# Kernel optimization log

Hardware: AMD Instinct MI355X
Metric: run time of the kernel (lower is better)

The kernel has to match this reference:

```python
import jax, jax.numpy as jnp
import numpy as np
import math

B, T, D, H = 4, 2048, 1024, 16
DH = D // H

def setup_inputs() -> dict:
    key = jax.random.key(0)
    ks = jax.random.split(key, 5)
    scale = 1.0 / math.sqrt(D)
    x = jax.random.normal(ks[0], (B, T, D), dtype=jnp.float32)
    Wq = jax.random.normal(ks[1], (D, D), dtype=jnp.float32) * scale
    Wk = jax.random.normal(ks[2], (D, D), dtype=jnp.float32) * scale
    Wv = jax.random.normal(ks[3], (D, D), dtype=jnp.float32) * scale
    Wo = jax.random.normal(ks[4], (D, D), dtype=jnp.float32) * scale
    mask = jnp.tril(jnp.ones((T, T), dtype=jnp.int32))  # causal, 1=keep
    return {"x": x, "mask": mask, "Wq": Wq, "Wk": Wk, "Wv": Wv, "Wo": Wo}

def reference(x, mask, Wq, Wk, Wv, Wo):
    Bx, Tx, Dx = x.shape
    # nn.Linear(bias=False): y = x @ W.T
    q = (x @ Wq.T).reshape(Bx, Tx, H, DH).transpose(0, 2, 1, 3)  # [B,H,T,dh]
    k = (x @ Wk.T).reshape(Bx, Tx, H, DH).transpose(0, 2, 1, 3)
    v = (x @ Wv.T).reshape(Bx, Tx, H, DH).transpose(0, 2, 1, 3)
    scores = jnp.einsum('bhqd,bhkd->bhqk', q, k) / math.sqrt(DH)
    m = mask[None, None, :, :]  # [1,1,T,T]
    scores = scores + (m == 0).astype(scores.dtype) * -1e9
    attn = jax.nn.softmax(scores, axis=-1)  # stable (max-subtract) like original
    out = jnp.einsum('bhqk,bhkd->bhqd', attn, v)
    out = out.transpose(0, 2, 1, 3).reshape(Bx, Tx, Dx)
    return out @ Wo.T
```

## Files before the change

### kernel.cpp

```cpp
#include <hip/hip_runtime.h>
#include <stdint.h>

#define B_  4
#define T_  2048
#define D_  1024
#define H_  16
#define DH_ 64

typedef unsigned short u16;
typedef __attribute__((ext_vector_type(8))) short bf16x8;
typedef __attribute__((ext_vector_type(8))) unsigned short u16x8;
typedef __attribute__((ext_vector_type(4))) unsigned short u16x4;
typedef __attribute__((ext_vector_type(4))) float f32x4;

#define NT_ ((size_t)B_ * T_ * D_)
#define QSCALE 0.18033688011112043f

__device__ __forceinline__ u16 f2bf(float f) {
    union { float f; uint32_t u; } v; v.f = f;
    uint32_t r = v.u + 0x7FFFu + ((v.u >> 16) & 1u);
    return (u16)(r >> 16);
}

__device__ __forceinline__ uint32_t pack2(float lo, float hi) {
    union { float f; uint32_t u; } a, b; a.f = lo; b.f = hi;
    return __builtin_amdgcn_perm(b.u, a.u, 0x07060302u);
}

__device__ __forceinline__ void gl2lds16(const u16* g, u16* l) {
    __builtin_amdgcn_global_load_lds(
        (const __attribute__((address_space(1))) unsigned int*)g,
        (__attribute__((address_space(3))) unsigned int*)l,
        16, 0, 0);
}

__global__ __launch_bounds__(256) void cvt_x_kernel(
    const float* __restrict__ src, u16* __restrict__ dst, int n8)
{
    int i = blockIdx.x * 256 + threadIdx.x;
    if (i >= n8) return;
    f32x4 a = ((const f32x4*)src)[2 * i];
    f32x4 b = ((const f32x4*)src)[2 * i + 1];
    u16x8 o;
    o[0]=f2bf(a[0]); o[1]=f2bf(a[1]); o[2]=f2bf(a[2]); o[3]=f2bf(a[3]);
    o[4]=f2bf(b[0]); o[5]=f2bf(b[1]); o[6]=f2bf(b[2]); o[7]=f2bf(b[3]);
    ((u16x8*)dst)[i] = o;
}

__global__ __launch_bounds__(256) void cvt_w_kernel(
    const float* __restrict__ w0, const float* __restrict__ w1,
    const float* __restrict__ w2, const float* __restrict__ w3,
    u16* __restrict__ dst)
{
    const float* src = (blockIdx.y == 0) ? w0 : (blockIdx.y == 1) ? w1
                     : (blockIdx.y == 2) ? w2 : w3;
    u16* d = dst + (size_t)blockIdx.y * (D_ * D_);
    int i = blockIdx.x * 256 + threadIdx.x;
    f32x4 a = ((const f32x4*)src)[2 * i];
    f32x4 b = ((const f32x4*)src)[2 * i + 1];
    u16x8 o;
    o[0]=f2bf(a[0]); o[1]=f2bf(a[1]); o[2]=f2bf(a[2]); o[3]=f2bf(a[3]);
    o[4]=f2bf(b[0]); o[5]=f2bf(b[1]); o[6]=f2bf(b[2]); o[7]=f2bf(b[3]);
    ((u16x8*)d)[i] = o;
}

template<int OUT_MODE>
__global__ __launch_bounds__(256) void gemm_bt_kernel(
    const u16* __restrict__ X, const u16* __restrict__ W,
    void* __restrict__ C, int M, int N, int K)
{
    __shared__ __align__(16) u16 As[128 * 64];
    __shared__ __align__(16) u16 Bs[128 * 64];

    const int tid  = threadIdx.x;
    const int wave = tid >> 6;
    const int lane = tid & 63;
    const int lq = lane >> 4;
    const int lm = lane & 15;
    const int m0 = blockIdx.x * 128;
    const int n0 = blockIdx.y * 128;
    const int wm = (wave & 1) * 64;
    const int wn = (wave >> 1) * 64;

    f32x4 acc[4][4] = {};

    const int r0 = wave * 32 + (lane >> 3);
    const int c0 = (lane & 7) * 8;
    const u16* gA = X + (size_t)(m0 + r0) * K + c0;
    const u16* gB = W + (size_t)(n0 + r0) * K + c0;
    u16* lA = As + wave * 32 * 64;
    u16* lB = Bs + wave * 32 * 64;

    for (int k0 = 0; k0 < K; k0 += 64) {
#pragma unroll
        for (int p = 0; p < 4; ++p) {
            gl2lds16(gA + (size_t)p * 8 * K + k0, lA + p * 8 * 64);
            gl2lds16(gB + (size_t)p * 8 * K + k0, lB + p * 8 * 64);
        }
        __syncthreads();
#pragma unroll
        for (int ks = 0; ks < 2; ++ks) {
            bf16x8 af[4], bfr[4];
#pragma unroll
            for (int t = 0; t < 4; ++t)
                af[t] = *(const bf16x8*)(As + (wm + t * 16 + lm) * 64 + ks * 32 + lq * 8);
#pragma unroll
            for (int t = 0; t < 4; ++t)
                bfr[t] = *(const bf16x8*)(Bs + (wn + t * 16 + lm) * 64 + ks * 32 + lq * 8);
#pragma unroll
            for (int i = 0; i < 4; ++i)
#pragma unroll
                for (int j = 0; j < 4; ++j)
                    acc[i][j] = __builtin_amdgcn_mfma_f32_16x16x32_bf16(
                        af[i], bfr[j], acc[i][j], 0, 0, 0);
        }
        __syncthreads();
    }

    const int region = n0 >> 10;
#pragma unroll
    for (int i = 0; i < 4; ++i)
#pragma unroll
        for (int j = 0; j < 4; ++j) {
            int rowb = m0 + wm + i * 16 + lq * 4;
            int col  = n0 + wn + j * 16 + lm;
            if (OUT_MODE == 2) {
#pragma unroll
                for (int r = 0; r < 4; ++r)
                    ((float*)C)[(size_t)(rowb + r) * N + col] = acc[i][j][r];
            } else {
                u16* Qp = (u16*)C;
                int colr = col & 1023;
                if (region == 0) {
#pragma unroll
                    for (int r = 0; r < 4; ++r)
                        Qp[(size_t)(rowb + r) * D_ + colr] = f2bf(acc[i][j][r] * QSCALE);
                } else if (region == 1) {
#pragma unroll
                    for (int r = 0; r < 4; ++r)
                        (Qp + NT_)[(size_t)(rowb + r) * D_ + colr] = f2bf(acc[i][j][r]);
                } else {
                    int b = rowb >> 11, t = rowb & (T_ - 1);
                    u16x4 pk;
#pragma unroll
                    for (int r = 0; r < 4; ++r) pk[r] = f2bf(acc[i][j][r]);
                    *(u16x4*)((Qp + 2 * NT_) + ((size_t)b * D_ + colr) * T_ + t) = pk;
                }
            }
        }
}

__global__ __launch_bounds__(64) void attn_kernel(
    const u16* __restrict__ Qg, const u16* __restrict__ Kg,
    const u16* __restrict__ Vtg, u16* __restrict__ Og)
{
    __shared__ __align__(16) u16 Pl[64 * 132];

    const int lane = threadIdx.x;
    const int lq = lane >> 4, lm = lane & 15;
    const int id = blockIdx.x;
    const int xs = id & 7;
    const int k8 = id >> 3;
    const int bh = xs + 8 * (k8 & 7);
    const int pi = k8 >> 3;
    const int b = bh >> 4, h = bh & 15;

    const size_t batchoff = (size_t)b * T_ * D_;
    const size_t headoff  = (size_t)h * DH_;
    const size_t vbase    = (size_t)bh * DH_ * T_;

#pragma unroll 1
    for (int ph = 0; ph < 2; ++ph) {
        const int qj  = ph ? (31 - pi) : pi;
        const int qw  = qj * 64;
        const int ktd = qj >> 1;
        const int odd = qj & 1;

        bf16x8 aq[4][2];
#pragma unroll
        for (int qf = 0; qf < 4; ++qf) {
            const u16* qrow = Qg + batchoff + (size_t)(qw + qf * 16 + lm) * D_ + headoff;
            aq[qf][0] = *(const bf16x8*)(qrow + lq * 8);
            aq[qf][1] = *(const bf16x8*)(qrow + 32 + lq * 8);
        }

        f32x4 oaccT[4][4] = {};
        float l_lane[4] = {0.f, 0.f, 0.f, 0.f};

#pragma unroll 1
        for (int kt = 0; kt <= ktd; ++kt) {
            const bool diag = (kt == ktd);
            const int ksmax = diag ? (odd ? 3 : 1) : 3;

#pragma unroll
            for (int c = 0; c < 4; ++c) {
                if (c <= ksmax) {
#pragma unroll
                    for (int t = 0; t < 2; ++t) {
                        const int mt = 2 * c + t;
                        const u16* krow = Kg + batchoff
                            + (size_t)(kt * 128 + mt * 16 + lm) * D_ + headoff;
                        bf16x8 kf0 = *(const bf16x8*)(krow + lq * 8);
                        bf16x8 kf1 = *(const bf16x8*)(krow + 32 + lq * 8);
                        f32x4 s[4];
#pragma unroll
                        for (int qf = 0; qf < 4; ++qf) {
                            s[qf] = f32x4{0.f, 0.f, 0.f, 0.f};
                            s[qf] = __builtin_amdgcn_mfma_f32_16x16x32_bf16(
                                kf0, aq[qf][0], s[qf], 0, 0, 0);
                            s[qf] = __builtin_amdgcn_mfma_f32_16x16x32_bf16(
                                kf1, aq[qf][1], s[qf], 0, 0, 0);
                        }
                        if (diag) {
                            int keyb = kt * 128 + mt * 16 + lq * 4;
#pragma unroll
                            for (int qf = 0; qf < 4; ++qf) {
                                int query = qw + qf * 16 + lm;
#pragma unroll
                                for (int r = 0; r < 4; ++r)
                                    if (keyb + r > query) s[qf][r] = -1e9f;
                            }
                        }
#pragma unroll
                        for (int qf = 0; qf < 4; ++qf) {
                            float p0 = __builtin_amdgcn_exp2f(s[qf][0]);
                            float p1 = __builtin_amdgcn_exp2f(s[qf][1]);
                            float p2 = __builtin_amdgcn_exp2f(s[qf][2]);
                            float p3 = __builtin_amdgcn_exp2f(s[qf][3]);
                            l_lane[qf] += (p0 + p1) + (p2 + p3);
                            uint2 d; d.x = pack2(p0, p1); d.y = pack2(p2, p3);
                            *(uint2*)(Pl + (qf * 16 + lm) * 132 + mt * 16 + lq * 4) = d;
                        }
                    }

                    bf16x8 pf[4];
#pragma unroll
                    for (int qf = 0; qf < 4; ++qf)
                        pf[qf] = *(const bf16x8*)(Pl + (qf * 16 + lm) * 132 + c * 32 + lq * 8);
#pragma unroll
                    for (int mo = 0; mo < 4; ++mo) {
                        const u16* vrow = Vtg + vbase
                            + (size_t)(mo * 16 + lm) * T_ + kt * 128 + c * 32;
                        bf16x8 vf = *(const bf16x8*)(vrow + lq * 8);
#pragma unroll
                        for (int qf = 0; qf < 4; ++qf)
                            oaccT[qf][mo] = __builtin_amdgcn_mfma_f32_16x16x32_bf16(
                                vf, pf[qf], oaccT[qf][mo], 0, 0, 0);
                    }
                }
            }
        }

#pragma unroll
        for (int qf = 0; qf < 4; ++qf) {
            float l = l_lane[qf];
            l += __shfl_xor(l, 16, 64);
            l += __shfl_xor(l, 32, 64);
            float inv = 1.0f / l;
            int row = qw + qf * 16 + lm;
            u16* obase = Og + batchoff + (size_t)row * D_ + headoff;
#pragma unroll
            for (int mo = 0; mo < 4; ++mo) {
                uint2 d;
                d.x = pack2(oaccT[qf][mo][0] * inv, oaccT[qf][mo][1] * inv);
                d.y = pack2(oaccT[qf][mo][2] * inv, oaccT[qf][mo][3] * inv);
                *(uint2*)(obase + mo * 16 + lq * 4) = d;
            }
        }
    }
}

extern "C" void kernel_launch(void* const* d_in, const int* in_sizes, int n_in,
                              void* d_out, int out_size, void* d_ws, size_t ws_size,
                              hipStream_t stream)
{
    const float* x  = (const float*)d_in[0];
    const float* Wq = (const float*)d_in[2];
    const float* Wk = (const float*)d_in[3];
    const float* Wv = (const float*)d_in[4];
    const float* Wo = (const float*)d_in[5];

    const size_t DD = (size_t)D_ * D_;
    u16* Qb  = (u16*)d_ws;
    u16* Kb  = Qb + NT_;
    u16* Vb  = Kb + NT_;
    u16* Ob  = Vb + NT_;
    u16* xb  = Ob + NT_;
    u16* wb  = xb + NT_;

    const int M = B_ * T_;

    cvt_x_kernel<<<dim3((int)(NT_ / 8 / 256)), 256, 0, stream>>>(x, xb, (int)(NT_ / 8));
    cvt_w_kernel<<<dim3((int)(DD / 8 / 256), 4), 256, 0, stream>>>(Wq, Wk, Wv, Wo, wb);

    gemm_bt_kernel<3><<<dim3(M / 128, 3 * D_ / 128), 256, 0, stream>>>(
        xb, wb, Qb, M, 3 * D_, D_);

    attn_kernel<<<dim3(1024), 64, 0, stream>>>(Qb, Kb, Vb, Ob);

    gemm_bt_kernel<2><<<dim3(M / 128, D_ / 128), 256, 0, stream>>>(
        Ob, wb + 3 * DD, d_out, M, D_, D_);
}
```

Measured before the change: 319.5 us.

## Split attention key tiles across two waves per block with LDS reduction

Each attention block now uses two waves that process alternating 128-key tiles for the same 64-query tile, then combine partial output accumulators and row sums through shared memory before normalizing and writing. The P staging buffer is shrunk to a per-wave 32-column slice. This doubles the parallelism per query tile and shortens the serial key loop, in exchange for extra LDS traffic, two barriers per phase, and more shared memory per block. It relies on the fixed-max softmax, where no running max is kept, so partial sums can simply be added.

```diff
diff --git a/kernel.cpp b/kernel.cpp
--- a/kernel.cpp
+++ b/kernel.cpp
@@ -150,13 +150,17 @@
         }
 }
 
-__global__ __launch_bounds__(64) void attn_kernel(
+__global__ __launch_bounds__(128) void attn_kernel(
     const u16* __restrict__ Qg, const u16* __restrict__ Kg,
     const u16* __restrict__ Vtg, u16* __restrict__ Og)
 {
-    __shared__ __align__(16) u16 Pl[64 * 132];
-
-    const int lane = threadIdx.x;
+    __shared__ __align__(16) u16 Pl[2 * 64 * 40];
+    __shared__ __align__(16) float Oc[16 * 64 * 4];
+    __shared__ __align__(16) float Lc[4 * 64];
+
+    const int tid  = threadIdx.x;
+    const int wave = tid >> 6;
+    const int lane = tid & 63;
     const int lq = lane >> 4, lm = lane & 15;
     const int id = blockIdx.x;
     const int xs = id & 7;
@@ -169,6 +173,8 @@
     const size_t headoff  = (size_t)h * DH_;
     const size_t vbase    = (size_t)bh * DH_ * T_;
 
+    u16* pw = Pl + wave * 64 * 40;
+
 #pragma unroll 1
     for (int ph = 0; ph < 2; ++ph) {
         const int qj  = ph ? (31 - pi) : pi;
@@ -188,7 +194,7 @@
         float l_lane[4] = {0.f, 0.f, 0.f, 0.f};
 
 #pragma unroll 1
-        for (int kt = 0; kt <= ktd; ++kt) {
+        for (int kt = wave; kt <= ktd; kt += 2) {
             const bool diag = (kt == ktd);
             const int ksmax = diag ? (odd ? 3 : 1) : 3;
 
@@ -229,14 +235,14 @@
                             float p3 = __builtin_amdgcn_exp2f(s[qf][3]);
                             l_lane[qf] += (p0 + p1) + (p2 + p3);
                             uint2 d; d.x = pack2(p0, p1); d.y = pack2(p2, p3);
-                            *(uint2*)(Pl + (qf * 16 + lm) * 132 + mt * 16 + lq * 4) = d;
+                            *(uint2*)(pw + (qf * 16 + lm) * 40 + t * 16 + lq * 4) = d;
                         }
                     }
 
                     bf16x8 pf[4];
 #pragma unroll
                     for (int qf = 0; qf < 4; ++qf)
-                        pf[qf] = *(const bf16x8*)(Pl + (qf * 16 + lm) * 132 + c * 32 + lq * 8);
+                        pf[qf] = *(const bf16x8*)(pw + (qf * 16 + lm) * 40 + lq * 8);
 #pragma unroll
                     for (int mo = 0; mo < 4; ++mo) {
                         const u16* vrow = Vtg + vbase
@@ -251,22 +257,45 @@
             }
         }
 
-#pragma unroll
-        for (int qf = 0; qf < 4; ++qf) {
-            float l = l_lane[qf];
-            l += __shfl_xor(l, 16, 64);
-            l += __shfl_xor(l, 32, 64);
-            float inv = 1.0f / l;
-            int row = qw + qf * 16 + lm;
-            u16* obase = Og + batchoff + (size_t)row * D_ + headoff;
-#pragma unroll
-            for (int mo = 0; mo < 4; ++mo) {
-                uint2 d;
-                d.x = pack2(oaccT[qf][mo][0] * inv, oaccT[qf][mo][1] * inv);
-                d.y = pack2(oaccT[qf][mo][2] * inv, oaccT[qf][mo][3] * inv);
-                *(uint2*)(obase + mo * 16 + lq * 4) = d;
-            }
-        }
+        if (wave == 1) {
+#pragma unroll
+            for (int qf = 0; qf < 4; ++qf) {
+#pragma unroll
+                for (int mo = 0; mo < 4; ++mo)
+                    *(f32x4*)&Oc[((qf * 4 + mo) * 64 + lane) * 4] = oaccT[qf][mo];
+                Lc[qf * 64 + lane] = l_lane[qf];
+            }
+        }
+        __syncthreads();
+        if (wave == 0) {
+#pragma unroll
+            for (int qf = 0; qf < 4; ++qf) {
+#pragma unroll
+                for (int mo = 0; mo < 4; ++mo) {
+                    f32x4 o = *(const f32x4*)&Oc[((qf * 4 + mo) * 64 + lane) * 4];
+#pragma unroll
+                    for (int r = 0; r < 4; ++r) oaccT[qf][mo][r] += o[r];
+                }
+                l_lane[qf] += Lc[qf * 64 + lane];
+            }
+#pragma unroll
+            for (int qf = 0; qf < 4; ++qf) {
+                float l = l_lane[qf];
+                l += __shfl_xor(l, 16, 64);
+                l += __shfl_xor(l, 32, 64);
+                float inv = 1.0f / l;
+                int row = qw + qf * 16 + lm;
+                u16* obase = Og + batchoff + (size_t)row * D_ + headoff;
+#pragma unroll
+                for (int mo = 0; mo < 4; ++mo) {
+                    uint2 d;
+                    d.x = pack2(oaccT[qf][mo][0] * inv, oaccT[qf][mo][1] * inv);
+                    d.y = pack2(oaccT[qf][mo][2] * inv, oaccT[qf][mo][3] * inv);
+                    *(uint2*)(obase + mo * 16 + lq * 4) = d;
+                }
+            }
+        }
+        __syncthreads();
     }
 }
 
@@ -296,7 +325,7 @@
     gemm_bt_kernel<3><<<dim3(M / 128, 3 * D_ / 128), 256, 0, stream>>>(
         xb, wb, Qb, M, 3 * D_, D_);
 
-    attn_kernel<<<dim3(1024), 64, 0, stream>>>(Qb, Kb, Vb, Ob);
+    attn_kernel<<<dim3(1024), 128, 0, stream>>>(Qb, Kb, Vb, Ob);
 
     gemm_bt_kernel<2><<<dim3(M / 128, D_ / 128), 256, 0, stream>>>(
         Ob, wb + 3 * DD, d_out, M, D_, D_);
```

Measured after the change: 288.9 us. -9.6%, faster.
